# Kernel optimization log

Measured on AMD Instinct MI355X. Metric: run time of the kernel, lower is better.

The kernel has to match this reference:

```python
import jax, jax.numpy as jnp
import numpy as np

N, D, F, E, TOP_K = 8192, 1024, 2048, 8, 2


def setup_inputs() -> dict:
    key = jax.random.key(0)
    ks = jax.random.split(key, 8)
    s = 0.02
    x = jax.random.normal(ks[0], (N, D), dtype=jnp.float32)
    Wr = jax.random.normal(ks[1], (D, E), dtype=jnp.float32) * s  # router
    br = jnp.zeros((E,), jnp.float32)
    W1 = jax.random.normal(ks[2], (E, D, F), dtype=jnp.float32) * s  # expert FFN in
    b1 = jnp.zeros((E, F), jnp.float32)
    W2 = jax.random.normal(ks[3], (E, F, D), dtype=jnp.float32) * s  # expert FFN out
    b2 = jnp.zeros((E, D), jnp. float32)
    return {"x": x, "Wr": Wr, "br": br, "W1": W1, "b1": b1, "W2": W2, "b2": b2}


def reference(x, Wr, br, W1, b1, W2, b2):
    # Router: per-token expert logits -> softmax probabilities -> top-k sampler.
    logits = x @ Wr + br                         # [N, E]
    probs = jax.nn.softmax(logits, axis=-1)      # [N, E]
    top_p, top_i = jax.lax.top_k(probs, TOP_K)   # [N, K]
    # Combine weights: prob mass only on the selected top-k experts per token.
    w = (jax.nn.one_hot(top_i, E, dtype=x.dtype) * top_p[..., None]).sum(axis=1)  # [N, E]
    # Per-expert gather-compute-scatter, expressed as masked full-batch expert FFN
    # (identical math: tokens not routed to expert e have weight 0).
    out = jnp.zeros((x.shape[0], W2.shape[-1]), dtype=x.dtype)
    for e in range(E):  # small fixed loop over structurally distinct experts
        h = jax.nn.gelu(x @ W1[e] + b1[e])       # [N, F]
        y = h @ W2[e] + b2[e]                    # [N, D]
        out = out + w[:, e:e + 1] * y            # weighted scatter-add combine
    return out
```

## Files before the change

### kernel.cpp

```cpp
#include <hip/hip_runtime.h>
#include <hip/hip_bf16.h>


#define N_TOK 8192
#define DIM   1024
#define FF    2048
#define NE    8

typedef unsigned short ushort_t;
typedef __bf16 bf16x8 __attribute__((ext_vector_type(8)));
typedef float  f32x4  __attribute__((ext_vector_type(4)));
typedef unsigned short u16x8 __attribute__((ext_vector_type(8)));

__device__ __forceinline__ ushort_t f2bf(float f) {
    union { float f; unsigned int u; } v; v.f = f;
    unsigned int r = (v.u + 0x7FFFu + ((v.u >> 16) & 1u)) >> 16;
    return (ushort_t)r;
}

__device__ __forceinline__ void gload_lds16(const ushort_t* g, ushort_t* l) {
    __builtin_amdgcn_global_load_lds(
        (const __attribute__((address_space(1))) void*)g,
        (__attribute__((address_space(3))) void*)l,
        16, 0, 0);
}

__global__ void transpose_conv_kernel(
    const float* __restrict__ in, ushort_t* __restrict__ out, int R, int C)
{
    __shared__ float tile[32][33];
    const int e = blockIdx.z;
    const float* I = in + (size_t)e * R * C;
    ushort_t*    O = out + (size_t)e * R * C;
    const int c0 = blockIdx.x * 32, r0 = blockIdx.y * 32;
    const int tx = threadIdx.x, ty = threadIdx.y;
#pragma unroll
    for (int j = 0; j < 32; j += 8)
        tile[ty + j][tx] = I[(size_t)(r0 + ty + j) * C + (c0 + tx)];
    __syncthreads();
#pragma unroll
    for (int j = 0; j < 32; j += 8)
        O[(size_t)(c0 + ty + j) * R + (r0 + tx)] = f2bf(tile[tx][ty + j]);
}

__global__ __launch_bounds__(256) void router_kernel(
    const float* __restrict__ x, const float* __restrict__ Wr, const float* __restrict__ br,
    int* __restrict__ cnt, int* __restrict__ tok_list, float* __restrict__ w_list)
{
    __shared__ int   se0[64], se1[64];
    __shared__ float sw0[64], sw1[64];

    const int wid  = threadIdx.x >> 6;
    const int lane = threadIdx.x & 63;
    const int tblk = blockIdx.x * 64;

    for (int i = 0; i < 16; ++i) {
        const int li = wid * 16 + i;
        const int t  = tblk + li;
        const float* xr = x + (size_t)t * DIM;

        float acc[NE];
#pragma unroll
        for (int e = 0; e < NE; ++e) acc[e] = 0.f;
        for (int d = lane; d < DIM; d += 64) {
            float xv = xr[d];
            const float4* w4 = reinterpret_cast<const float4*>(Wr + (size_t)d * NE);
            float4 w0 = w4[0], w1 = w4[1];
            acc[0] += xv * w0.x; acc[1] += xv * w0.y; acc[2] += xv * w0.z; acc[3] += xv * w0.w;
            acc[4] += xv * w1.x; acc[5] += xv * w1.y; acc[6] += xv * w1.z; acc[7] += xv * w1.w;
        }
#pragma unroll
        for (int e = 0; e < NE; ++e) {
            for (int off = 32; off > 0; off >>= 1)
                acc[e] += __shfl_down(acc[e], off, 64);
        }
        if (lane == 0) {
            float l[NE];
#pragma unroll
            for (int e = 0; e < NE; ++e) l[e] = acc[e] + br[e];
            float mx = l[0];
#pragma unroll
            for (int e = 1; e < NE; ++e) mx = fmaxf(mx, l[e]);
            float p[NE], s = 0.f;
#pragma unroll
            for (int e = 0; e < NE; ++e) { p[e] = expf(l[e] - mx); s += p[e]; }
            float inv = 1.f / s;
            int e0 = 0;
#pragma unroll
            for (int e = 1; e < NE; ++e) if (l[e] > l[e0]) e0 = e;
            int e1 = (e0 == 0) ? 1 : 0;
#pragma unroll
            for (int e = 0; e < NE; ++e) if (e != e0 && l[e] > l[e1]) e1 = e;
            se0[li] = e0; sw0[li] = p[e0] * inv;
            se1[li] = e1; sw1[li] = p[e1] * inv;
        }
    }
    __syncthreads();

    if (threadIdx.x < 64) {
        const int t  = tblk + lane;
        const int e0 = se0[lane], e1 = se1[lane];
        const unsigned long long below = ((unsigned long long)1 << lane) - 1;
        int p0 = 0, p1 = 0;
#pragma unroll
        for (int e = 0; e < NE; ++e) {
            unsigned long long m0 = __ballot(e0 == e);
            unsigned long long m1 = __ballot(e1 == e);
            int c = __popcll(m0) + __popcll(m1);
            int b = 0;
            if (lane == e && c) b = atomicAdd(&cnt[e], c);
            b = __shfl(b, e, 64);
            if (e0 == e) p0 = b + __popcll(m0 & below);
            if (e1 == e) p1 = b + __popcll(m0) + __popcll(m1 & below);
        }
        tok_list[e0 * N_TOK + p0] = t;  w_list[e0 * N_TOK + p0] = sw0[lane];
        tok_list[e1 * N_TOK + p1] = t;  w_list[e1 * N_TOK + p1] = sw1[lane];
    }
}

__global__ void scan_kernel(const int* __restrict__ cnt, int* __restrict__ offs)
{
    if (threadIdx.x == 0 && blockIdx.x == 0) {
        int s = 0;
        for (int e = 0; e < NE; ++e) { offs[e] = s; s += cnt[e]; }
        offs[NE] = s;
    }
}

__global__ __launch_bounds__(256) void gather_a_kernel(
    const float* __restrict__ x, const int* __restrict__ offs,
    const int* __restrict__ tok_list, ushort_t* __restrict__ xpack)
{
    const int c   = blockIdx.x * 256 + threadIdx.x;
    const int row = c >> 7;
    int e = 0;
#pragma unroll
    for (int k = 1; k < NE; ++k) e += (row >= offs[k]);
    const int tok = tok_list[e * N_TOK + (row - offs[e])];
    const int d0  = (c & 127) << 3;
    const float* src = x + ((size_t)tok << 10) + d0;
    float4 a = *reinterpret_cast<const float4*>(src);
    float4 b = *reinterpret_cast<const float4*>(src + 4);
    u16x8 o;
    o[0] = f2bf(a.x); o[1] = f2bf(a.y); o[2] = f2bf(a.z); o[3] = f2bf(a.w);
    o[4] = f2bf(b.x); o[5] = f2bf(b.y); o[6] = f2bf(b.z); o[7] = f2bf(b.w);
    *reinterpret_cast<u16x8*>(xpack + ((size_t)row << 10) + d0) = o;
}

template <int MODE>
__global__ __launch_bounds__(256) void moe_gemm_kernel(
    const ushort_t* __restrict__ A,
    const ushort_t* __restrict__ Bt,
    const float*    __restrict__ bias,
    const int*      __restrict__ cnt,
    const int*      __restrict__ offs,
    const int*      __restrict__ tok_list,
    const float*    __restrict__ w_list,
    ushort_t*       __restrict__ hout,
    float*          __restrict__ out,
    int K, int NCOL)
{
    const int e = blockIdx.z;
    const int cnt_e = cnt[e];

    const int cpx = gridDim.x >> 3;
    const int wg  = (blockIdx.x & 7) * cpx + (blockIdx.x >> 3);
    const int mb  = wg & 63;
    const int nb  = wg >> 6;

    const int m0 = mb * 128;
    if (m0 >= cnt_e) return;
    const int n0 = nb * 128;
    const int offs_e = offs[e];

    __shared__ ushort_t As[3][128 * 32];
    __shared__ ushort_t Bs[3][128 * 32];

    const int tid = threadIdx.x;

    size_t asrc[2], bsrc[2];
#pragma unroll
    for (int j = 0; j < 2; ++j) {
        int c = tid + 256 * j;
        int row   = c >> 2;
        int chunk = (c & 3) ^ ((row >> 1) & 3);
        int entry = m0 + row;
        size_t arow;
        if (MODE == 0) {
            arow = (entry < cnt_e) ? (size_t)(offs_e + entry) * K : 0;
        } else {
            arow = (size_t)(offs_e + entry) * K;
        }
        asrc[j] = arow + (size_t)chunk * 8;
        int col = n0 + row;
        bsrc[j] = ((size_t)e * NCOL + col) * K + (size_t)chunk * 8;
    }

    f32x4 acc[4][4];
#pragma unroll
    for (int m = 0; m < 4; ++m)
#pragma unroll
        for (int n = 0; n < 4; ++n)
            acc[m][n] = (f32x4){0.f, 0.f, 0.f, 0.f};

    const int lane = tid & 63;
    const int wid  = tid >> 6;
    const int wr = (wid >> 1) * 64;
    const int wc = (wid & 1) * 64;
    const int la = lane & 15;
    const int kc = lane >> 4;

    auto STAGE = [&](int t, int b) {
        int k0 = t * 32;
#pragma unroll
        for (int j = 0; j < 2; ++j) {
            gload_lds16(A  + asrc[j] + k0, &As[b][(tid + 256 * j) * 8]);
            gload_lds16(Bt + bsrc[j] + k0, &Bs[b][(tid + 256 * j) * 8]);
        }
    };

    auto COMPUTE = [&](int b) {
        bf16x8 af[4], bfr[4];
#pragma unroll
        for (int m = 0; m < 4; ++m) {
            int r = wr + m * 16 + la;
            af[m] = *reinterpret_cast<const bf16x8*>(&As[b][(r * 4 + (kc ^ ((r >> 1) & 3))) * 8]);
        }
#pragma unroll
        for (int n = 0; n < 4; ++n) {
            int r = wc + n * 16 + la;
            bfr[n] = *reinterpret_cast<const bf16x8*>(&Bs[b][(r * 4 + (kc ^ ((r >> 1) & 3))) * 8]);
        }
#pragma unroll
        for (int m = 0; m < 4; ++m)
#pragma unroll
            for (int n = 0; n < 4; ++n)
                acc[m][n] = __builtin_amdgcn_mfma_f32_16x16x32_bf16(af[m], bfr[n], acc[m][n], 0, 0, 0);
    };

    const int nk = K / 32;
    STAGE(0, 0);
    STAGE(1, 1);
    for (int t = 0; t < nk - 1; ++t) {
        asm volatile("s_waitcnt vmcnt(4)" ::: "memory");
        __builtin_amdgcn_s_barrier();
        if (t + 2 < nk) STAGE(t + 2, (t + 2) % 3);
        COMPUTE(t % 3);
    }
    asm volatile("s_waitcnt vmcnt(0)" ::: "memory");
    __builtin_amdgcn_s_barrier();
    COMPUTE((nk - 1) % 3);

#pragma unroll
    for (int m = 0; m < 4; ++m) {
        int rbase = wr + m * 16 + (lane >> 4) * 4;
#pragma unroll
        for (int n = 0; n < 4; ++n) {
            int gcol = n0 + wc + n * 16 + la;
            float bi = bias[(size_t)e * NCOL + gcol];
#pragma unroll
            for (int jj = 0; jj < 4; ++jj) {
                int entry = m0 + rbase + jj;
                if (entry < cnt_e) {
                    float v = acc[m][n][jj] + bi;
                    if (MODE == 0) {
                        float u = 0.7978845608028654f * (v + 0.044715f * v * v * v);
                        float g = 0.5f * v * (1.f + tanhf(u));
                        hout[(size_t)(offs_e + entry) * NCOL + gcol] = f2bf(g);
                    } else {
                        int tok  = tok_list[e * N_TOK + entry];
                        float w  = w_list  [e * N_TOK + entry];
                        atomicAdd(&out[(size_t)tok * NCOL + gcol], w * v);
                    }
                }
            }
        }
    }
}

extern "C" void kernel_launch(void* const* d_in, const int* in_sizes, int n_in,
                              void* d_out, int out_size, void* d_ws, size_t ws_size,
                              hipStream_t stream)
{
    const float* x  = (const float*)d_in[0];
    const float* Wr = (const float*)d_in[1];
    const float* br = (const float*)d_in[2];
    const float* W1 = (const float*)d_in[3];
    const float* b1 = (const float*)d_in[4];
    const float* W2 = (const float*)d_in[5];
    const float* b2 = (const float*)d_in[6];
    float* out = (float*)d_out;

    char* ws = (char*)d_ws;
    size_t off = 0;
    auto alloc = [&](size_t bytes) -> void* {
        void* p = ws + off;
        off = (off + bytes + 255) & ~(size_t)255;
        return p;
    };
    ushort_t* w1t = (ushort_t*)alloc((size_t)NE * DIM * FF * 2);
    ushort_t* w2t = (ushort_t*)alloc((size_t)NE * DIM * FF * 2);
    ushort_t* xpack = (ushort_t*)alloc((size_t)2 * N_TOK * DIM * 2);
    ushort_t* h   = (ushort_t*)alloc(((size_t)2 * N_TOK + 128) * FF * 2);
    int*      cnt = (int*)alloc(NE * sizeof(int));
    int*      offs= (int*)alloc((NE + 1) * sizeof(int));
    int*   tok_list = (int*)alloc((size_t)NE * N_TOK * sizeof(int));
    float* w_list   = (float*)alloc((size_t)NE * N_TOK * sizeof(float));
    (void)ws_size; (void)in_sizes; (void)n_in;

    hipMemsetAsync(out, 0, (size_t)out_size * sizeof(float), stream);
    hipMemsetAsync(cnt, 0, NE * sizeof(int), stream);

    transpose_conv_kernel<<<dim3(FF / 32, DIM / 32, NE), dim3(32, 8), 0, stream>>>(W1, w1t, DIM, FF);
    transpose_conv_kernel<<<dim3(DIM / 32, FF / 32, NE), dim3(32, 8), 0, stream>>>(W2, w2t, FF, DIM);
    router_kernel<<<N_TOK / 64, 256, 0, stream>>>(x, Wr, br, cnt, tok_list, w_list);
    scan_kernel<<<1, 64, 0, stream>>>(cnt, offs);
    gather_a_kernel<<<(2 * N_TOK * DIM) / (8 * 256), 256, 0, stream>>>(x, offs, tok_list, xpack);

    moe_gemm_kernel<0><<<dim3(64 * (FF / 128), 1, NE), 256, 0, stream>>>(
        xpack, w1t, b1, cnt, offs, tok_list, w_list, h, nullptr, DIM, FF);
    moe_gemm_kernel<1><<<dim3(64 * (DIM / 128), 1, NE), 256, 0, stream>>>(
        h, w2t, b2, cnt, offs, tok_list, w_list, nullptr, out, FF, DIM);
}
```

Measured before the change: 527.4 us.

## Use persistent grouped-GEMM scheduling over compact tile list, widen transpose tiles

```diff
diff --git a/kernel.cpp b/kernel.cpp
--- a/kernel.cpp
+++ b/kernel.cpp
@@ -25,22 +25,32 @@
         16, 0, 0);
 }
 
-__global__ void transpose_conv_kernel(
+__global__ __launch_bounds__(256) void transpose_conv_kernel(
     const float* __restrict__ in, ushort_t* __restrict__ out, int R, int C)
 {
-    __shared__ float tile[32][33];
+    __shared__ float tile[64][68];
     const int e = blockIdx.z;
     const float* I = in + (size_t)e * R * C;
     ushort_t*    O = out + (size_t)e * R * C;
-    const int c0 = blockIdx.x * 32, r0 = blockIdx.y * 32;
-    const int tx = threadIdx.x, ty = threadIdx.y;
-#pragma unroll
-    for (int j = 0; j < 32; j += 8)
-        tile[ty + j][tx] = I[(size_t)(r0 + ty + j) * C + (c0 + tx)];
+    const int c0 = blockIdx.x * 64, r0 = blockIdx.y * 64;
+    const int tid = threadIdx.x;
+#pragma unroll
+    for (int j = 0; j < 4; ++j) {
+        int row = j * 16 + (tid >> 4);
+        int col = (tid & 15) * 4;
+        float4 v = *reinterpret_cast<const float4*>(&I[(size_t)(r0 + row) * C + c0 + col]);
+        *reinterpret_cast<float4*>(&tile[row][col]) = v;
+    }
     __syncthreads();
 #pragma unroll
-    for (int j = 0; j < 32; j += 8)
-        O[(size_t)(c0 + ty + j) * R + (r0 + tx)] = f2bf(tile[tx][ty + j]);
+    for (int j = 0; j < 2; ++j) {
+        int orow = j * 32 + (tid >> 3);
+        int k0   = (tid & 7) * 8;
+        u16x8 o;
+#pragma unroll
+        for (int k = 0; k < 8; ++k) o[k] = f2bf(tile[k0 + k][orow]);
+        *reinterpret_cast<u16x8*>(&O[(size_t)(c0 + orow) * R + r0 + k0]) = o;
+    }
 }
 
 __global__ __launch_bounds__(256) void router_kernel(
@@ -118,12 +128,20 @@
     }
 }
 
-__global__ void scan_kernel(const int* __restrict__ cnt, int* __restrict__ offs)
+__global__ void scan_kernel(const int* __restrict__ cnt, int* __restrict__ offs,
+                            int* __restrict__ tile_e, int* __restrict__ tile_m0,
+                            int* __restrict__ meta)
 {
     if (threadIdx.x == 0 && blockIdx.x == 0) {
         int s = 0;
         for (int e = 0; e < NE; ++e) { offs[e] = s; s += cnt[e]; }
         offs[NE] = s;
+        int nt = 0;
+        for (int e = 0; e < NE; ++e)
+            for (int m0 = 0; m0 < cnt[e]; m0 += 128) {
+                tile_e[nt] = e; tile_m0[nt] = m0; ++nt;
+            }
+        meta[0] = nt;
     }
 }
 
@@ -156,53 +174,26 @@
     const int*      __restrict__ offs,
     const int*      __restrict__ tok_list,
     const float*    __restrict__ w_list,
+    const int*      __restrict__ tile_e,
+    const int*      __restrict__ tile_m0,
+    const int*      __restrict__ meta,
     ushort_t*       __restrict__ hout,
     float*          __restrict__ out,
     int K, int NCOL)
 {
-    const int e = blockIdx.z;
-    const int cnt_e = cnt[e];
-
-    const int cpx = gridDim.x >> 3;
-    const int wg  = (blockIdx.x & 7) * cpx + (blockIdx.x >> 3);
-    const int mb  = wg & 63;
-    const int nb  = wg >> 6;
-
-    const int m0 = mb * 128;
-    if (m0 >= cnt_e) return;
-    const int n0 = nb * 128;
-    const int offs_e = offs[e];
+    const int nmt = meta[0];
+    const int NB  = NCOL >> 7;
+    const int L   = nmt * NB;
+
+    const int xcd = blockIdx.x & 7;
+    const int q = L >> 3, r = L & 7;
+    const int cstart = (xcd < r) ? xcd * (q + 1) : r * (q + 1) + (xcd - r) * q;
+    const int clen   = (xcd < r) ? q + 1 : q;
 
     __shared__ ushort_t As[3][128 * 32];
     __shared__ ushort_t Bs[3][128 * 32];
 
-    const int tid = threadIdx.x;
-
-    size_t asrc[2], bsrc[2];
-#pragma unroll
-    for (int j = 0; j < 2; ++j) {
-        int c = tid + 256 * j;
-        int row   = c >> 2;
-        int chunk = (c & 3) ^ ((row >> 1) & 3);
-        int entry = m0 + row;
-        size_t arow;
-        if (MODE == 0) {
-            arow = (entry < cnt_e) ? (size_t)(offs_e + entry) * K : 0;
-        } else {
-            arow = (size_t)(offs_e + entry) * K;
-        }
-        asrc[j] = arow + (size_t)chunk * 8;
-        int col = n0 + row;
-        bsrc[j] = ((size_t)e * NCOL + col) * K + (size_t)chunk * 8;
-    }
-
-    f32x4 acc[4][4];
-#pragma unroll
-    for (int m = 0; m < 4; ++m)
-#pragma unroll
-        for (int n = 0; n < 4; ++n)
-            acc[m][n] = (f32x4){0.f, 0.f, 0.f, 0.f};
-
+    const int tid  = threadIdx.x;
     const int lane = tid & 63;
     const int wid  = tid >> 6;
     const int wr = (wid >> 1) * 64;
@@ -210,67 +201,107 @@
     const int la = lane & 15;
     const int kc = lane >> 4;
 
-    auto STAGE = [&](int t, int b) {
-        int k0 = t * 32;
+    for (int i = blockIdx.x >> 3; i < clen; i += 96) {
+        const int tau = cstart + i;
+        const int nb  = tau & (NB - 1);
+        const int mt  = tau >> (NB == 16 ? 4 : 3);
+        const int e   = tile_e[mt];
+        const int m0  = tile_m0[mt];
+        const int cnt_e  = cnt[e];
+        const int offs_e = offs[e];
+        const int n0  = nb * 128;
+
+        __syncthreads();
+
+        size_t asrc[2], bsrc[2];
 #pragma unroll
         for (int j = 0; j < 2; ++j) {
-            gload_lds16(A  + asrc[j] + k0, &As[b][(tid + 256 * j) * 8]);
-            gload_lds16(Bt + bsrc[j] + k0, &Bs[b][(tid + 256 * j) * 8]);
-        }
-    };
-
-    auto COMPUTE = [&](int b) {
-        bf16x8 af[4], bfr[4];
+            int c = tid + 256 * j;
+            int row   = c >> 2;
+            int chunk = (c & 3) ^ ((row >> 1) & 3);
+            int entry = m0 + row;
+            size_t arow;
+            if (MODE == 0) {
+                arow = (entry < cnt_e) ? (size_t)(offs_e + entry) * K : 0;
+            } else {
+                arow = (size_t)(offs_e + entry) * K;
+            }
+            asrc[j] = arow + (size_t)chunk * 8;
+            int col = n0 + row;
+            bsrc[j] = ((size_t)e * NCOL + col) * K + (size_t)chunk * 8;
+        }
+
+        f32x4 acc[4][4];
+#pragma unroll
+        for (int m = 0; m < 4; ++m)
+#pragma unroll
+            for (int n = 0; n < 4; ++n)
+                acc[m][n] = (f32x4){0.f, 0.f, 0.f, 0.f};
+
+        auto STAGE = [&](int t, int b) {
+            int k0 = t * 32;
+#pragma unroll
+            for (int j = 0; j < 2; ++j) {
+                gload_lds16(A  + asrc[j] + k0, &As[b][(tid + 256 * j) * 8]);
+                gload_lds16(Bt + bsrc[j] + k0, &Bs[b][(tid + 256 * j) * 8]);
+            }
+        };
+
+        auto COMPUTE = [&](int b) {
+            bf16x8 af[4], bfr[4];
+#pragma unroll
+            for (int m = 0; m < 4; ++m) {
+                int rr = wr + m * 16 + la;
+                af[m] = *reinterpret_cast<const bf16x8*>(&As[b][(rr * 4 + (kc ^ ((rr >> 1) & 3))) * 8]);
+            }
+#pragma unroll
+            for (int n = 0; n < 4; ++n) {
+                int rr = wc + n * 16 + la;
+                bfr[n] = *reinterpret_cast<const bf16x8*>(&Bs[b][(rr * 4 + (kc ^ ((rr >> 1) & 3))) * 8]);
+            }
+            __builtin_amdgcn_s_setprio(1);
+#pragma unroll
+            for (int m = 0; m < 4; ++m)
+#pragma unroll
+                for (int n = 0; n < 4; ++n)
+                    acc[m][n] = __builtin_amdgcn_mfma_f32_16x16x32_bf16(af[m], bfr[n], acc[m][n], 0, 0, 0);
+            __builtin_amdgcn_s_setprio(0);
+        };
+
+        const int nk = K / 32;
+        STAGE(0, 0);
+        STAGE(1, 1);
+        for (int t = 0; t < nk - 1; ++t) {
+            asm volatile("s_waitcnt vmcnt(4)" ::: "memory");
+            __builtin_amdgcn_s_barrier();
+            if (t + 2 < nk) STAGE(t + 2, (t + 2) % 3);
+            COMPUTE(t % 3);
+        }
+        asm volatile("s_waitcnt vmcnt(0)" ::: "memory");
+        __builtin_amdgcn_s_barrier();
+        COMPUTE((nk - 1) % 3);
+
 #pragma unroll
         for (int m = 0; m < 4; ++m) {
-            int r = wr + m * 16 + la;
-            af[m] = *reinterpret_cast<const bf16x8*>(&As[b][(r * 4 + (kc ^ ((r >> 1) & 3))) * 8]);
-        }
-#pragma unroll
-        for (int n = 0; n < 4; ++n) {
-            int r = wc + n * 16 + la;
-            bfr[n] = *reinterpret_cast<const bf16x8*>(&Bs[b][(r * 4 + (kc ^ ((r >> 1) & 3))) * 8]);
-        }
-#pragma unroll
-        for (int m = 0; m < 4; ++m)
-#pragma unroll
-            for (int n = 0; n < 4; ++n)
-                acc[m][n] = __builtin_amdgcn_mfma_f32_16x16x32_bf16(af[m], bfr[n], acc[m][n], 0, 0, 0);
-    };
-
-    const int nk = K / 32;
-    STAGE(0, 0);
-    STAGE(1, 1);
-    for (int t = 0; t < nk - 1; ++t) {
-        asm volatile("s_waitcnt vmcnt(4)" ::: "memory");
-        __builtin_amdgcn_s_barrier();
-        if (t + 2 < nk) STAGE(t + 2, (t + 2) % 3);
-        COMPUTE(t % 3);
-    }
-    asm volatile("s_waitcnt vmcnt(0)" ::: "memory");
-    __builtin_amdgcn_s_barrier();
-    COMPUTE((nk - 1) % 3);
-
-#pragma unroll
-    for (int m = 0; m < 4; ++m) {
-        int rbase = wr + m * 16 + (lane >> 4) * 4;
-#pragma unroll
-        for (int n = 0; n < 4; ++n) {
-            int gcol = n0 + wc + n * 16 + la;
-            float bi = bias[(size_t)e * NCOL + gcol];
-#pragma unroll
-            for (int jj = 0; jj < 4; ++jj) {
-                int entry = m0 + rbase + jj;
-                if (entry < cnt_e) {
-                    float v = acc[m][n][jj] + bi;
-                    if (MODE == 0) {
-                        float u = 0.7978845608028654f * (v + 0.044715f * v * v * v);
-                        float g = 0.5f * v * (1.f + tanhf(u));
-                        hout[(size_t)(offs_e + entry) * NCOL + gcol] = f2bf(g);
-                    } else {
-                        int tok  = tok_list[e * N_TOK + entry];
-                        float w  = w_list  [e * N_TOK + entry];
-                        atomicAdd(&out[(size_t)tok * NCOL + gcol], w * v);
+            int rbase = wr + m * 16 + (lane >> 4) * 4;
+#pragma unroll
+            for (int n = 0; n < 4; ++n) {
+                int gcol = n0 + wc + n * 16 + la;
+                float bi = bias[(size_t)e * NCOL + gcol];
+#pragma unroll
+                for (int jj = 0; jj < 4; ++jj) {
+                    int entry = m0 + rbase + jj;
+                    if (entry < cnt_e) {
+                        float v = acc[m][n][jj] + bi;
+                        if (MODE == 0) {
+                            float u = 0.7978845608028654f * (v + 0.044715f * v * v * v);
+                            float g = 0.5f * v * (1.f + tanhf(u));
+                            hout[(size_t)(offs_e + entry) * NCOL + gcol] = f2bf(g);
+                        } else {
+                            int tok  = tok_list[e * N_TOK + entry];
+                            float w  = w_list  [e * N_TOK + entry];
+                            atomicAdd(&out[(size_t)tok * NCOL + gcol], w * v);
+                        }
                     }
                 }
             }
@@ -301,24 +332,27 @@
     ushort_t* w1t = (ushort_t*)alloc((size_t)NE * DIM * FF * 2);
     ushort_t* w2t = (ushort_t*)alloc((size_t)NE * DIM * FF * 2);
     ushort_t* xpack = (ushort_t*)alloc((size_t)2 * N_TOK * DIM * 2);
-    ushort_t* h   = (ushort_t*)alloc(((size_t)2 * N_TOK + 128) * FF * 2);
+    ushort_t* h   = (ushort_t*)alloc(((size_t)2 * N_TOK + 256) * FF * 2);
     int*      cnt = (int*)alloc(NE * sizeof(int));
     int*      offs= (int*)alloc((NE + 1) * sizeof(int));
     int*   tok_list = (int*)alloc((size_t)NE * N_TOK * sizeof(int));
     float* w_list   = (float*)alloc((size_t)NE * N_TOK * sizeof(float));
+    int*   tile_e   = (int*)alloc(256 * sizeof(int));
+    int*   tile_m0  = (int*)alloc(256 * sizeof(int));
+    int*   meta     = (int*)alloc(16 * sizeof(int));
     (void)ws_size; (void)in_sizes; (void)n_in;
 
     hipMemsetAsync(out, 0, (size_t)out_size * sizeof(float), stream);
     hipMemsetAsync(cnt, 0, NE * sizeof(int), stream);
 
-    transpose_conv_kernel<<<dim3(FF / 32, DIM / 32, NE), dim3(32, 8), 0, stream>>>(W1, w1t, DIM, FF);
-    transpose_conv_kernel<<<dim3(DIM / 32, FF / 32, NE), dim3(32, 8), 0, stream>>>(W2, w2t, FF, DIM);
+    transpose_conv_kernel<<<dim3(FF / 64, DIM / 64, NE), 256, 0, stream>>>(W1, w1t, DIM, FF);
+    transpose_conv_kernel<<<dim3(DIM / 64, FF / 64, NE), 256, 0, stream>>>(W2, w2t, FF, DIM);
     router_kernel<<<N_TOK / 64, 256, 0, stream>>>(x, Wr, br, cnt, tok_list, w_list);
-    scan_kernel<<<1, 64, 0, stream>>>(cnt, offs);
+    scan_kernel<<<1, 64, 0, stream>>>(cnt, offs, tile_e, tile_m0, meta);
     gather_a_kernel<<<(2 * N_TOK * DIM) / (8 * 256), 256, 0, stream>>>(x, offs, tok_list, xpack);
 
-    moe_gemm_kernel<0><<<dim3(64 * (FF / 128), 1, NE), 256, 0, stream>>>(
-        xpack, w1t, b1, cnt, offs, tok_list, w_list, h, nullptr, DIM, FF);
-    moe_gemm_kernel<1><<<dim3(64 * (DIM / 128), 1, NE), 256, 0, stream>>>(
-        h, w2t, b2, cnt, offs, tok_list, w_list, nullptr, out, FF, DIM);
-}
+    moe_gemm_kernel<0><<<768, 256, 0, stream>>>(
+        xpack, w1t, b1, cnt, offs, tok_list, w_list, tile_e, tile_m0, meta, h, nullptr, DIM, FF);
+    moe_gemm_kernel<1><<<768, 256, 0, stream>>>(
+        h, w2t, b2, cnt, offs, tok_list, w_list, tile_e, tile_m0, meta, nullptr, out, FF, DIM);
+}
```

Measured after the change: 504.6 us. 1.05x faster.
